# Optimization experiments

Measured on AMD Instinct MI355X. Metric: run time of the kernel, lower is better.

The kernel has to match this reference:

```python
import jax, jax.numpy as jnp
import numpy as np

D_MODEL = 768
NHEAD = 12
D_K = D_MODEL // NHEAD
D_FF = 3072
EPS = 1e-6


def layer_norm(x, a, b):
    # torch LayerNorm here: mean/std over last dim, std is UNBIASED (n-1), eps added to std
    n = x.shape[-1]
    m = jnp.mean(x, axis=-1, keepdims=True)
    var = jnp.sum((x - m) ** 2, axis=-1, keepdims=True) / (n - 1)
    return a * (x - m) / (jnp.sqrt(var) + EPS) + b


def setup_inputs() -> dict:
    key = jax.random.key(0)
    ks = jax.random.split(key, 12)
    B, S = 2, 2048
    s = 1.0 / np.sqrt(D_MODEL)
    inp = {
        'x': jax.random.normal(ks[0], (B, S, D_MODEL), jnp.float32),
        'mask': jnp.ones((B, 1, S), jnp.int32),
        'Wq': jax.random.normal(ks[1], (D_MODEL, D_MODEL), jnp.float32) * s,
        'bq': jnp.zeros((D_MODEL,), jnp.float32),
        'Wk': jax.random.normal(ks[2], (D_MODEL, D_MODEL), jnp.float32) * s,
        'bk': jnp.zeros((D_MODEL,), jnp.float32),
        'Wv': jax.random.normal(ks[3], (D_MODEL, D_MODEL), jnp.float32) * s,
        'bv': jnp.zeros((D_MODEL,), jnp.float32),
        'Wo': jax.random.normal(ks[4], (D_MODEL, D_MODEL), jnp.float32) * s,
        'bo': jnp.zeros((D_MODEL,), jnp.float32),
        'ln1_a': jnp.ones((D_MODEL,), jnp.float32),
        'ln1_b': jnp.zeros((D_MODEL,), jnp.float32),
        'W1': jax.random.normal(ks[5], (D_MODEL, D_FF), jnp.float32) * s,
        'b1': jnp.zeros((D_FF,), jnp.float32),
        'W2': jax.random.normal(ks[6], (D_FF, D_MODEL), jnp.float32) * (1.0 / np.sqrt(D_FF)),
        'b2': jnp.zeros((D_MODEL,), jnp.float32),
        'ln2_a': jnp.ones((D_MODEL,), jnp.float32),
        'ln2_b': jnp.zeros((D_MODEL,), jnp.float32),
    }
    return inp


def reference(x, mask, Wq, bq, Wk, bk, Wv, bv, Wo, bo, ln1_a, ln1_b, W1, b1, W2, b2, ln2_a, ln2_b):
    B, S, _ = x.shape
    # --- sublayer 1: pre-norm self-attention + residual (dropout = eval/no-op) ---
    h = layer_norm(x, ln1_a, ln1_b)
    q = (h @ Wq + bq).reshape(B, S, NHEAD, D_K).transpose(0, 2, 1, 3)  # [B,H,S,Dk]
    k = (h @ Wk + bk).reshape(B, S, NHEAD, D_K).transpose(0, 2, 1, 3)
    v = (h @ Wv + bv).reshape(B, S, NHEAD, D_K).transpose(0, 2, 1, 3)
    scores = jnp.einsum('bhqd,bhkd->bhqk', q, k) / np.sqrt(D_K)  # [B,H,S,S]
    scores = jnp.where(mask[:, None] == 0, jnp.float32(-1e9), scores)
    attn = jax.nn.softmax(scores, axis=-1)
    ctx = jnp.einsum('bhqk,bhkd->bhqd', attn, v)  # [B,H,S,Dk]
    ctx = ctx.transpose(0, 2, 1, 3).reshape(B, S, D_MODEL)
    x = x + (ctx @ Wo + bo)
    # --- sublayer 2: pre-norm FFN + residual ---
    h2 = layer_norm(x, ln2_a, ln2_b)
    ff = jax.nn.relu(h2 @ W1 + b1) @ W2 + b2
    return x + ff
```

## Files before the change

kernel.cpp:

```cpp
#include <hip/hip_runtime.h>
#include <hip/hip_bf16.h>
#include <stdint.h>

#define DM 768
#define DFF 3072
#define NH 12
#define DK 64
#define SS 2048
#define NTOK 4096

typedef __hip_bfloat16 bf16;
typedef short bf16x8 __attribute__((ext_vector_type(8)));
typedef float f32x4 __attribute__((ext_vector_type(4)));

#define MFMA16(a, b, c) __builtin_amdgcn_mfma_f32_16x16x32_bf16((a), (b), (c), 0, 0, 0)

static __device__ __forceinline__ bf16 f2b(float f) { return __float2bfloat16(f); }
static __device__ __forceinline__ unsigned short f2b_bits(float f) {
    bf16 h = __float2bfloat16(f);
    return *reinterpret_cast<unsigned short*>(&h);
}

static __device__ __forceinline__ void g2l16(const void* g, void* l) {
    __builtin_amdgcn_global_load_lds(
        (const __attribute__((address_space(1))) unsigned int*)g,
        (__attribute__((address_space(3))) unsigned int*)(uintptr_t)l,
        16, 0, 0);
}

__global__ __launch_bounds__(256) void transpose_cvt(const float* __restrict__ W,
                                                     bf16* __restrict__ WT,
                                                     int K, int N) {
    __shared__ float tile[32][33];
    int n0 = blockIdx.x * 32, k0 = blockIdx.y * 32;
    int tx = threadIdx.x & 31, ty = threadIdx.x >> 5;
#pragma unroll
    for (int r = ty; r < 32; r += 8)
        tile[r][tx] = W[(size_t)(k0 + r) * N + n0 + tx];
    __syncthreads();
#pragma unroll
    for (int r = ty; r < 32; r += 8)
        WT[(size_t)(n0 + r) * K + k0 + tx] = f2b(tile[tx][r]);
}

__global__ __launch_bounds__(256) void transpose_cvt4(const float* W0, const float* W1,
                                                      const float* W2, const float* W3,
                                                      bf16* T0, bf16* T1, bf16* T2, bf16* T3) {
    __shared__ float tile[32][33];
    const float* W = (blockIdx.z == 0) ? W0 : (blockIdx.z == 1) ? W1 : (blockIdx.z == 2) ? W2 : W3;
    bf16* WT = (blockIdx.z == 0) ? T0 : (blockIdx.z == 1) ? T1 : (blockIdx.z == 2) ? T2 : T3;
    int n0 = blockIdx.x * 32, k0 = blockIdx.y * 32;
    int tx = threadIdx.x & 31, ty = threadIdx.x >> 5;
#pragma unroll
    for (int r = ty; r < 32; r += 8)
        tile[r][tx] = W[(size_t)(k0 + r) * DM + n0 + tx];
    __syncthreads();
#pragma unroll
    for (int r = ty; r < 32; r += 8)
        WT[(size_t)(n0 + r) * DM + k0 + tx] = f2b(tile[tx][r]);
}

__global__ __launch_bounds__(256) void ln_fwd(const float* __restrict__ x,
                                              const float* __restrict__ g,
                                              const float* __restrict__ be,
                                              bf16* __restrict__ out) {
    int wid = threadIdx.x >> 6, lane = threadIdx.x & 63;
    int row = blockIdx.x * 4 + wid;
    const float* xr = x + (size_t)row * DM;
    float v[12];
    float s = 0.f;
#pragma unroll
    for (int i = 0; i < 12; ++i) { v[i] = xr[lane + i * 64]; s += v[i]; }
#pragma unroll
    for (int off = 32; off >= 1; off >>= 1) s += __shfl_xor(s, off);
    float mean = s * (1.f / 768.f);
    float s2 = 0.f;
#pragma unroll
    for (int i = 0; i < 12; ++i) { float d = v[i] - mean; s2 += d * d; }
#pragma unroll
    for (int off = 32; off >= 1; off >>= 1) s2 += __shfl_xor(s2, off);
    float rstd = 1.f / (sqrtf(s2 * (1.f / 767.f)) + 1e-6f);
    bf16* orow = out + (size_t)row * DM;
#pragma unroll
    for (int i = 0; i < 12; ++i) {
        int c = lane + i * 64;
        orow[c] = f2b(g[c] * (v[i] - mean) * rstd + be[c]);
    }
}

__device__ __forceinline__ void gemm_core(const bf16* __restrict__ A,
                                          const bf16* __restrict__ BT,
                                          int K, int bm, int bn,
                                          bf16* As, bf16* Bs,
                                          f32x4 acc[4][4]) {
    int tid = threadIdx.x;
    int lane = tid & 63, quad = lane >> 4, lid = lane & 15;
    int wid = tid >> 6;
    int wm = (wid >> 1) * 64, wn = (wid & 1) * 64;
    int s0 = tid, s1 = tid + 256;
    int r0 = s0 >> 2, c0 = (s0 & 3) ^ ((r0 >> 1) & 3);
    int r1 = s1 >> 2, c1 = (s1 & 3) ^ ((r1 >> 1) & 3);
    const bf16* A0 = A + (size_t)(bm + r0) * K + c0 * 8;
    const bf16* A1 = A + (size_t)(bm + r1) * K + c1 * 8;
    const bf16* B0 = BT + (size_t)(bn + r0) * K + c0 * 8;
    const bf16* B1 = BT + (size_t)(bn + r1) * K + c1 * 8;
    int rdc = quad ^ ((lid >> 1) & 3);
    for (int k0 = 0; k0 < K; k0 += 32) {
        __syncthreads();
        g2l16(A0 + k0, As + s0 * 8);
        g2l16(B0 + k0, Bs + s0 * 8);
        g2l16(A1 + k0, As + s1 * 8);
        g2l16(B1 + k0, Bs + s1 * 8);
        __syncthreads();
        bf16x8 af[4], bfr[4];
#pragma unroll
        for (int i = 0; i < 4; ++i) af[i]  = *(const bf16x8*)&As[(wm + i * 16 + lid) * 32 + rdc * 8];
#pragma unroll
        for (int j = 0; j < 4; ++j) bfr[j] = *(const bf16x8*)&Bs[(wn + j * 16 + lid) * 32 + rdc * 8];
#pragma unroll
        for (int i = 0; i < 4; ++i)
#pragma unroll
            for (int j = 0; j < 4; ++j)
                acc[i][j] = MFMA16(af[i], bfr[j], acc[i][j]);
    }
}

__global__ __launch_bounds__(256) void gemm_qkv(const bf16* __restrict__ A,
                                                const bf16* __restrict__ WqT,
                                                const bf16* __restrict__ WkT,
                                                const bf16* __restrict__ WvT,
                                                const float* __restrict__ bq,
                                                const float* __restrict__ bk,
                                                const float* __restrict__ bv,
                                                bf16* __restrict__ qb,
                                                bf16* __restrict__ kb,
                                                bf16* __restrict__ vtb) {
    __shared__ bf16 As[128 * 32];
    __shared__ bf16 Bs[128 * 32];
    int which = blockIdx.x / 6;
    int bn = (blockIdx.x % 6) * 128;
    int bm = blockIdx.y * 128;
    const bf16* BT = (which == 0) ? WqT : (which == 1) ? WkT : WvT;
    const float* bias = (which == 0) ? bq : (which == 1) ? bk : bv;
    f32x4 acc[4][4] = {};
    gemm_core(A, BT, DM, bm, bn, As, Bs, acc);

    int tid = threadIdx.x, wid = tid >> 6, lane = tid & 63, quad = lane >> 4, lid = lane & 15;
    int wm = (wid >> 1) * 64, wn = (wid & 1) * 64;
#pragma unroll
    for (int j = 0; j < 4; ++j) {
        int col = bn + wn + j * 16 + lid;
        float bb = bias[col];
        int hh = col >> 6, d = col & 63;
#pragma unroll
        for (int i = 0; i < 4; ++i) {
            int rowbase = bm + wm + i * 16 + quad * 4;
            int b = rowbase >> 11;
            int s0 = rowbase & 2047;
            if (which == 2) {
                ushort4 pk;
                pk.x = f2b_bits(acc[i][j][0] + bb);
                pk.y = f2b_bits(acc[i][j][1] + bb);
                pk.z = f2b_bits(acc[i][j][2] + bb);
                pk.w = f2b_bits(acc[i][j][3] + bb);
                *(ushort4*)&vtb[(((size_t)b * NH + hh) * DK + d) * SS + s0] = pk;
            } else {
                bf16* dst = which ? kb : qb;
#pragma unroll
                for (int r = 0; r < 4; ++r)
                    dst[(((size_t)b * NH + hh) * SS + (s0 + r)) * DK + d] = f2b(acc[i][j][r] + bb);
            }
        }
    }
}

template <int EPI>
__global__ __launch_bounds__(256) void gemm_ep(const bf16* __restrict__ A,
                                               const bf16* __restrict__ BT,
                                               const float* __restrict__ bias,
                                               const float* __restrict__ res,
                                               void* __restrict__ outp,
                                               int N, int K) {
    __shared__ bf16 As[128 * 32];
    __shared__ bf16 Bs[128 * 32];
    int bm = blockIdx.y * 128, bn = blockIdx.x * 128;
    f32x4 acc[4][4] = {};
    gemm_core(A, BT, K, bm, bn, As, Bs, acc);

    int tid = threadIdx.x, wid = tid >> 6, lane = tid & 63, quad = lane >> 4, lid = lane & 15;
    int wm = (wid >> 1) * 64, wn = (wid & 1) * 64;
#pragma unroll
    for (int j = 0; j < 4; ++j) {
        int col = bn + wn + j * 16 + lid;
        float bb = bias[col];
#pragma unroll
        for (int i = 0; i < 4; ++i) {
#pragma unroll
            for (int r = 0; r < 4; ++r) {
                int row = bm + wm + i * 16 + quad * 4 + r;
                float v = acc[i][j][r] + bb;
                if (EPI == 2) {
                    ((float*)outp)[(size_t)row * N + col] = res[(size_t)row * N + col] + v;
                } else {
                    ((bf16*)outp)[(size_t)row * N + col] = f2b(fmaxf(v, 0.f));
                }
            }
        }
    }
}

template <int EPI>
__global__ __launch_bounds__(256) void gemm_ep64(const bf16* __restrict__ A,
                                                 const bf16* __restrict__ BT,
                                                 const float* __restrict__ bias,
                                                 const float* __restrict__ res,
                                                 void* __restrict__ outp,
                                                 int N, int K) {
    __shared__ bf16 As[64 * 32];
    __shared__ bf16 Bs[128 * 32];
    int bm = blockIdx.y * 64, bn = blockIdx.x * 128;
    int tid = threadIdx.x, wid = tid >> 6, lane = tid & 63, quad = lane >> 4, lid = lane & 15;
    int wm = (wid >> 1) * 32, wn = (wid & 1) * 64;
    f32x4 acc[2][4] = {};
    int ra = tid >> 2, ca = (tid & 3) ^ ((ra >> 1) & 3);
    int s0 = tid, s1 = tid + 256;
    int rb0 = s0 >> 2, cb0 = (s0 & 3) ^ ((rb0 >> 1) & 3);
    int rb1 = s1 >> 2, cb1 = (s1 & 3) ^ ((rb1 >> 1) & 3);
    const bf16* Ap = A + (size_t)(bm + ra) * K + ca * 8;
    const bf16* B0 = BT + (size_t)(bn + rb0) * K + cb0 * 8;
    const bf16* B1 = BT + (size_t)(bn + rb1) * K + cb1 * 8;
    int rdc = quad ^ ((lid >> 1) & 3);
    for (int k0 = 0; k0 < K; k0 += 32) {
        __syncthreads();
        g2l16(Ap + k0, As + tid * 8);
        g2l16(B0 + k0, Bs + s0 * 8);
        g2l16(B1 + k0, Bs + s1 * 8);
        __syncthreads();
        bf16x8 af[2], bfr[4];
#pragma unroll
        for (int i = 0; i < 2; ++i) af[i]  = *(const bf16x8*)&As[(wm + i * 16 + lid) * 32 + rdc * 8];
#pragma unroll
        for (int j = 0; j < 4; ++j) bfr[j] = *(const bf16x8*)&Bs[(wn + j * 16 + lid) * 32 + rdc * 8];
#pragma unroll
        for (int i = 0; i < 2; ++i)
#pragma unroll
            for (int j = 0; j < 4; ++j)
                acc[i][j] = MFMA16(af[i], bfr[j], acc[i][j]);
    }
#pragma unroll
    for (int j = 0; j < 4; ++j) {
        int col = bn + wn + j * 16 + lid;
        float bb = bias[col];
#pragma unroll
        for (int i = 0; i < 2; ++i) {
#pragma unroll
            for (int r = 0; r < 4; ++r) {
                int row = bm + wm + i * 16 + quad * 4 + r;
                float v = acc[i][j][r] + bb;
                if (EPI == 2) {
                    ((float*)outp)[(size_t)row * N + col] = res[(size_t)row * N + col] + v;
                } else {
                    ((bf16*)outp)[(size_t)row * N + col] = f2b(fmaxf(v, 0.f));
                }
            }
        }
    }
}

__global__ __launch_bounds__(256) void attn_fwd(const bf16* __restrict__ qb,
                                                const bf16* __restrict__ kb,
                                                const bf16* __restrict__ vtb,
                                                const int* __restrict__ mask,
                                                bf16* __restrict__ ctx) {
    __shared__ bf16 Qs[64 * 64];
    __shared__ bf16 Ks[2][64 * 64];
    __shared__ bf16 VTs[2][64 * 64];
    __shared__ bf16 Ps[64 * 72];
    int bh = blockIdx.y;
    int b = bh / NH, h = bh % NH;
    int q0 = blockIdx.x * 64;
    const bf16* Q  = qb  + (size_t)bh * SS * DK;
    const bf16* Kp = kb  + (size_t)bh * SS * DK;
    const bf16* VT = vtb + (size_t)bh * DK * SS;
    int tid = threadIdx.x, wid = tid >> 6, lane = tid & 63, quad = lane >> 4, lid = lane & 15;

    int s0 = tid, s1 = tid + 256;
    int r0 = s0 >> 3, c0 = (s0 & 7) ^ (r0 & 7);
    int r1 = s1 >> 3, c1 = (s1 & 7) ^ (r1 & 7);
    g2l16(Q + (size_t)(q0 + r0) * DK + c0 * 8, Qs + s0 * 8);
    g2l16(Q + (size_t)(q0 + r1) * DK + c1 * 8, Qs + s1 * 8);
    g2l16(Kp + (size_t)r0 * DK + c0 * 8, Ks[0] + s0 * 8);
    g2l16(Kp + (size_t)r1 * DK + c1 * 8, Ks[0] + s1 * 8);
    g2l16(VT + (size_t)r0 * SS + c0 * 8, VTs[0] + s0 * 8);
    g2l16(VT + (size_t)r1 * SS + c1 * 8, VTs[0] + s1 * 8);

    int rdc  = quad ^ (lid & 7);
    int rdc2 = rdc ^ 4;

    f32x4 accv[4] = {};
    float l_part[4] = {0.f, 0.f, 0.f, 0.f};

    for (int t = 0; t < SS / 64; ++t) {
        __syncthreads();
        int cur = t & 1;
        if (t + 1 < SS / 64) {
            int k1 = (t + 1) * 64;
            g2l16(Kp + (size_t)(k1 + r0) * DK + c0 * 8, Ks[cur ^ 1] + s0 * 8);
            g2l16(Kp + (size_t)(k1 + r1) * DK + c1 * 8, Ks[cur ^ 1] + s1 * 8);
            g2l16(VT + (size_t)r0 * SS + k1 + c0 * 8, VTs[cur ^ 1] + s0 * 8);
            g2l16(VT + (size_t)r1 * SS + k1 + c1 * 8, VTs[cur ^ 1] + s1 * 8);
        }
        int k0 = t * 64;
        const bf16* Kc = Ks[cur];
        const bf16* Vc = VTs[cur];

        int mk[4];
#pragma unroll
        for (int ns = 0; ns < 4; ++ns) mk[ns] = mask[b * SS + k0 + ns * 16 + lid];

#pragma unroll
        for (int ns = 0; ns < 4; ++ns) {
            f32x4 sa = {};
            sa = MFMA16(*(const bf16x8*)&Qs[(wid * 16 + lid) * 64 + rdc * 8],
                        *(const bf16x8*)&Kc[(ns * 16 + lid) * 64 + rdc * 8], sa);
            sa = MFMA16(*(const bf16x8*)&Qs[(wid * 16 + lid) * 64 + rdc2 * 8],
                        *(const bf16x8*)&Kc[(ns * 16 + lid) * 64 + rdc2 * 8], sa);
#pragma unroll
            for (int r = 0; r < 4; ++r) {
                float pv = mk[ns] ? __expf(sa[r] * 0.125f) : 0.f;
                Ps[(wid * 16 + quad * 4 + r) * 72 + ns * 16 + lid] = f2b(pv);
                l_part[r] += pv;
            }
        }

#pragma unroll
        for (int ds = 0; ds < 4; ++ds) {
            accv[ds] = MFMA16(*(const bf16x8*)&Ps[(wid * 16 + lid) * 72 + quad * 8],
                              *(const bf16x8*)&Vc[(ds * 16 + lid) * 64 + rdc * 8], accv[ds]);
            accv[ds] = MFMA16(*(const bf16x8*)&Ps[(wid * 16 + lid) * 72 + 32 + quad * 8],
                              *(const bf16x8*)&Vc[(ds * 16 + lid) * 64 + rdc2 * 8], accv[ds]);
        }
    }

#pragma unroll
    for (int r = 0; r < 4; ++r) {
#pragma unroll
        for (int off = 8; off >= 1; off >>= 1) l_part[r] += __shfl_xor(l_part[r], off);
    }

#pragma unroll
    for (int ds = 0; ds < 4; ++ds) {
#pragma unroll
        for (int r = 0; r < 4; ++r) {
            int row = q0 + wid * 16 + quad * 4 + r;
            int col = h * DK + ds * 16 + lid;
            ctx[(size_t)(b * SS + row) * DM + col] = f2b(accv[ds][r] / l_part[r]);
        }
    }
}

extern "C" void kernel_launch(void* const* d_in, const int* in_sizes, int n_in,
                              void* d_out, int out_size, void* d_ws, size_t ws_size,
                              hipStream_t stream) {
    const float* x    = (const float*)d_in[0];
    const int*   mask = (const int*)d_in[1];
    const float* Wq   = (const float*)d_in[2];
    const float* bq   = (const float*)d_in[3];
    const float* Wk   = (const float*)d_in[4];
    const float* bk   = (const float*)d_in[5];
    const float* Wv   = (const float*)d_in[6];
    const float* bv   = (const float*)d_in[7];
    const float* Wo   = (const float*)d_in[8];
    const float* bo   = (const float*)d_in[9];
    const float* ln1a = (const float*)d_in[10];
    const float* ln1b = (const float*)d_in[11];
    const float* W1   = (const float*)d_in[12];
    const float* b1   = (const float*)d_in[13];
    const float* W2   = (const float*)d_in[14];
    const float* b2   = (const float*)d_in[15];
    const float* ln2a = (const float*)d_in[16];
    const float* ln2b = (const float*)d_in[17];
    float* out = (float*)d_out;

    char* w = (char*)d_ws;
    bf16* h   = (bf16*)w; w += (size_t)NTOK * DM * 2;
    bf16* qb  = (bf16*)w; w += (size_t)NTOK * DM * 2;
    bf16* kb  = (bf16*)w; w += (size_t)NTOK * DM * 2;
    bf16* vtb = (bf16*)w; w += (size_t)NTOK * DM * 2;
    bf16* ctx = (bf16*)w; w += (size_t)NTOK * DM * 2;
    bf16* h2  = (bf16*)w; w += (size_t)NTOK * DM * 2;
    bf16* ffa = (bf16*)w; w += (size_t)NTOK * DFF * 2;
    float* x1 = (float*)w; w += (size_t)NTOK * DM * 4;
    bf16* WqT = (bf16*)w; w += (size_t)DM * DM * 2;
    bf16* WkT = (bf16*)w; w += (size_t)DM * DM * 2;
    bf16* WvT = (bf16*)w; w += (size_t)DM * DM * 2;
    bf16* WoT = (bf16*)w; w += (size_t)DM * DM * 2;
    bf16* W1T = (bf16*)w; w += (size_t)DM * DFF * 2;
    bf16* W2T = (bf16*)w; w += (size_t)DM * DFF * 2;

    transpose_cvt4<<<dim3(24, 24, 4), 256, 0, stream>>>(Wq, Wk, Wv, Wo, WqT, WkT, WvT, WoT);
    transpose_cvt<<<dim3(96, 24), 256, 0, stream>>>(W1, W1T, DM, DFF);
    transpose_cvt<<<dim3(24, 96), 256, 0, stream>>>(W2, W2T, DFF, DM);

    ln_fwd<<<NTOK / 4, 256, 0, stream>>>(x, ln1a, ln1b, h);
    gemm_qkv<<<dim3(18, 32), 256, 0, stream>>>(h, WqT, WkT, WvT, bq, bk, bv, qb, kb, vtb);
    attn_fwd<<<dim3(SS / 64, 2 * NH), 256, 0, stream>>>(qb, kb, vtb, mask, ctx);
    gemm_ep64<2><<<dim3(6, 64), 256, 0, stream>>>(ctx, WoT, bo, x, (void*)x1, DM, DM);
    ln_fwd<<<NTOK / 4, 256, 0, stream>>>(x1, ln2a, ln2b, h2);
    gemm_ep<3><<<dim3(24, 32), 256, 0, stream>>>(h2, W1T, b1, nullptr, (void*)ffa, DFF, DM);
    gemm_ep64<2><<<dim3(6, 64), 256, 0, stream>>>(ffa, W2T, b2, x1, (void*)out, DM, DFF);
}
```

Before: 319.4 us.

## Double-buffer GEMM LDS tiles and keep attention probabilities in registers

The GEMM cores now double-buffer their shared-memory tiles, prefetching the next K slice while computing the current one, which drops one barrier per iteration. The attention kernel computes transposed scores (K·Qᵀ) so the probability fragments land directly in the B-operand layout of a 16x16x16 MFMA. This removes the P round-trip through LDS. Q is pre-scaled by log2(e)/sqrt(dk) in the QKV epilogue so exp2f replaces expf plus a multiply. LDS usage for the GEMMs doubles, which may lower occupancy, and the attention path depends on a K16 bf16 MFMA builtin being available.

```diff
diff --git a/kernel.cpp b/kernel.cpp
--- a/kernel.cpp
+++ b/kernel.cpp
@@ -10,10 +10,23 @@
 #define NTOK 4096
 
 typedef __hip_bfloat16 bf16;
+typedef short bf16x4 __attribute__((ext_vector_type(4)));
 typedef short bf16x8 __attribute__((ext_vector_type(8)));
 typedef float f32x4 __attribute__((ext_vector_type(4)));
 
 #define MFMA16(a, b, c) __builtin_amdgcn_mfma_f32_16x16x32_bf16((a), (b), (c), 0, 0, 0)
+
+#if __has_builtin(__builtin_amdgcn_mfma_f32_16x16x16bf16_1k)
+#define HAVE_K16 1
+#define MFMA_K16(a, b, c) __builtin_amdgcn_mfma_f32_16x16x16bf16_1k((a), (b), (c), 0, 0, 0)
+#elif __has_builtin(__builtin_amdgcn_mfma_f32_16x16x16_bf16)
+#define HAVE_K16 1
+#define MFMA_K16(a, b, c) __builtin_amdgcn_mfma_f32_16x16x16_bf16((a), (b), (c), 0, 0, 0)
+#else
+#define HAVE_K16 0
+#endif
+
+#define QSCALE 0.18033688011112042f
 
 static __device__ __forceinline__ bf16 f2b(float f) { return __float2bfloat16(f); }
 static __device__ __forceinline__ unsigned short f2b_bits(float f) {
@@ -105,18 +118,27 @@
     const bf16* B0 = BT + (size_t)(bn + r0) * K + c0 * 8;
     const bf16* B1 = BT + (size_t)(bn + r1) * K + c1 * 8;
     int rdc = quad ^ ((lid >> 1) & 3);
+    g2l16(A0, As + s0 * 8);
+    g2l16(B0, Bs + s0 * 8);
+    g2l16(A1, As + s1 * 8);
+    g2l16(B1, Bs + s1 * 8);
     for (int k0 = 0; k0 < K; k0 += 32) {
         __syncthreads();
-        g2l16(A0 + k0, As + s0 * 8);
-        g2l16(B0 + k0, Bs + s0 * 8);
-        g2l16(A1 + k0, As + s1 * 8);
-        g2l16(B1 + k0, Bs + s1 * 8);
-        __syncthreads();
+        int cur = (k0 >> 5) & 1;
+        if (k0 + 32 < K) {
+            int nb = (cur ^ 1) * 4096;
+            g2l16(A0 + k0 + 32, As + nb + s0 * 8);
+            g2l16(B0 + k0 + 32, Bs + nb + s0 * 8);
+            g2l16(A1 + k0 + 32, As + nb + s1 * 8);
+            g2l16(B1 + k0 + 32, Bs + nb + s1 * 8);
+        }
+        const bf16* Ac = As + cur * 4096;
+        const bf16* Bc = Bs + cur * 4096;
         bf16x8 af[4], bfr[4];
 #pragma unroll
-        for (int i = 0; i < 4; ++i) af[i]  = *(const bf16x8*)&As[(wm + i * 16 + lid) * 32 + rdc * 8];
-#pragma unroll
-        for (int j = 0; j < 4; ++j) bfr[j] = *(const bf16x8*)&Bs[(wn + j * 16 + lid) * 32 + rdc * 8];
+        for (int i = 0; i < 4; ++i) af[i]  = *(const bf16x8*)&Ac[(wm + i * 16 + lid) * 32 + rdc * 8];
+#pragma unroll
+        for (int j = 0; j < 4; ++j) bfr[j] = *(const bf16x8*)&Bc[(wn + j * 16 + lid) * 32 + rdc * 8];
 #pragma unroll
         for (int i = 0; i < 4; ++i)
 #pragma unroll
@@ -135,8 +157,8 @@
                                                 bf16* __restrict__ qb,
                                                 bf16* __restrict__ kb,
                                                 bf16* __restrict__ vtb) {
-    __shared__ bf16 As[128 * 32];
-    __shared__ bf16 Bs[128 * 32];
+    __shared__ bf16 As[2 * 128 * 32];
+    __shared__ bf16 Bs[2 * 128 * 32];
     int which = blockIdx.x / 6;
     int bn = (blockIdx.x % 6) * 128;
     int bm = blockIdx.y * 128;
@@ -147,6 +169,7 @@
 
     int tid = threadIdx.x, wid = tid >> 6, lane = tid & 63, quad = lane >> 4, lid = lane & 15;
     int wm = (wid >> 1) * 64, wn = (wid & 1) * 64;
+    float sc = (which == 0) ? QSCALE : 1.f;
 #pragma unroll
     for (int j = 0; j < 4; ++j) {
         int col = bn + wn + j * 16 + lid;
@@ -168,7 +191,7 @@
                 bf16* dst = which ? kb : qb;
 #pragma unroll
                 for (int r = 0; r < 4; ++r)
-                    dst[(((size_t)b * NH + hh) * SS + (s0 + r)) * DK + d] = f2b(acc[i][j][r] + bb);
+                    dst[(((size_t)b * NH + hh) * SS + (s0 + r)) * DK + d] = f2b((acc[i][j][r] + bb) * sc);
             }
         }
     }
@@ -181,8 +204,8 @@
                                                const float* __restrict__ res,
                                                void* __restrict__ outp,
                                                int N, int K) {
-    __shared__ bf16 As[128 * 32];
-    __shared__ bf16 Bs[128 * 32];
+    __shared__ bf16 As[2 * 128 * 32];
+    __shared__ bf16 Bs[2 * 128 * 32];
     int bm = blockIdx.y * 128, bn = blockIdx.x * 128;
     f32x4 acc[4][4] = {};
     gemm_core(A, BT, K, bm, bn, As, Bs, acc);
@@ -216,8 +239,8 @@
                                                  const float* __restrict__ res,
                                                  void* __restrict__ outp,
                                                  int N, int K) {
-    __shared__ bf16 As[64 * 32];
-    __shared__ bf16 Bs[128 * 32];
+    __shared__ bf16 As[2 * 64 * 32];
+    __shared__ bf16 Bs[2 * 128 * 32];
     int bm = blockIdx.y * 64, bn = blockIdx.x * 128;
     int tid = threadIdx.x, wid = tid >> 6, lane = tid & 63, quad = lane >> 4, lid = lane & 15;
     int wm = (wid >> 1) * 32, wn = (wid & 1) * 64;
@@ -230,17 +253,24 @@
     const bf16* B0 = BT + (size_t)(bn + rb0) * K + cb0 * 8;
     const bf16* B1 = BT + (size_t)(bn + rb1) * K + cb1 * 8;
     int rdc = quad ^ ((lid >> 1) & 3);
+    g2l16(Ap, As + tid * 8);
+    g2l16(B0, Bs + s0 * 8);
+    g2l16(B1, Bs + s1 * 8);
     for (int k0 = 0; k0 < K; k0 += 32) {
         __syncthreads();
-        g2l16(Ap + k0, As + tid * 8);
-        g2l16(B0 + k0, Bs + s0 * 8);
-        g2l16(B1 + k0, Bs + s1 * 8);
-        __syncthreads();
+        int cur = (k0 >> 5) & 1;
+        if (k0 + 32 < K) {
+            g2l16(Ap + k0 + 32, As + (cur ^ 1) * 2048 + tid * 8);
+            g2l16(B0 + k0 + 32, Bs + (cur ^ 1) * 4096 + s0 * 8);
+            g2l16(B1 + k0 + 32, Bs + (cur ^ 1) * 4096 + s1 * 8);
+        }
+        const bf16* Ac = As + cur * 2048;
+        const bf16* Bc = Bs + cur * 4096;
         bf16x8 af[2], bfr[4];
 #pragma unroll
-        for (int i = 0; i < 2; ++i) af[i]  = *(const bf16x8*)&As[(wm + i * 16 + lid) * 32 + rdc * 8];
-#pragma unroll
-        for (int j = 0; j < 4; ++j) bfr[j] = *(const bf16x8*)&Bs[(wn + j * 16 + lid) * 32 + rdc * 8];
+        for (int i = 0; i < 2; ++i) af[i]  = *(const bf16x8*)&Ac[(wm + i * 16 + lid) * 32 + rdc * 8];
+#pragma unroll
+        for (int j = 0; j < 4; ++j) bfr[j] = *(const bf16x8*)&Bc[(wn + j * 16 + lid) * 32 + rdc * 8];
 #pragma unroll
         for (int i = 0; i < 2; ++i)
 #pragma unroll
@@ -267,12 +297,106 @@
     }
 }
 
+#if HAVE_K16
 __global__ __launch_bounds__(256) void attn_fwd(const bf16* __restrict__ qb,
                                                 const bf16* __restrict__ kb,
                                                 const bf16* __restrict__ vtb,
                                                 const int* __restrict__ mask,
                                                 bf16* __restrict__ ctx) {
-    __shared__ bf16 Qs[64 * 64];
+    __shared__ bf16 Ks[2][64 * 64];
+    __shared__ bf16 VTs[2][64 * 64];
+    int bh = blockIdx.y;
+    int b = bh / NH, h = bh % NH;
+    int q0 = blockIdx.x * 64;
+    const bf16* Q  = qb  + (size_t)bh * SS * DK;
+    const bf16* Kp = kb  + (size_t)bh * SS * DK;
+    const bf16* VT = vtb + (size_t)bh * DK * SS;
+    int tid = threadIdx.x, wid = tid >> 6, lane = tid & 63, quad = lane >> 4, lid = lane & 15;
+
+    int s0 = tid, s1 = tid + 256;
+    int r0 = s0 >> 3, c0 = (s0 & 7) ^ (r0 & 7);
+    int r1 = s1 >> 3, c1 = (s1 & 7) ^ (r1 & 7);
+    g2l16(Kp + (size_t)r0 * DK + c0 * 8, Ks[0] + s0 * 8);
+    g2l16(Kp + (size_t)r1 * DK + c1 * 8, Ks[0] + s1 * 8);
+    g2l16(VT + (size_t)r0 * SS + c0 * 8, VTs[0] + s0 * 8);
+    g2l16(VT + (size_t)r1 * SS + c1 * 8, VTs[0] + s1 * 8);
+
+    const bf16* Qrow = Q + (size_t)(q0 + wid * 16 + lid) * DK;
+    bf16x8 qf0 = *(const bf16x8*)&Qrow[quad * 8];
+    bf16x8 qf1 = *(const bf16x8*)&Qrow[32 + quad * 8];
+
+    int rdc  = quad ^ (lid & 7);
+    int rdc2 = rdc ^ 4;
+    const int* mrow = mask + b * SS;
+
+    f32x4 accv[4] = {};
+    float l_part = 0.f;
+
+    for (int t = 0; t < SS / 64; ++t) {
+        __syncthreads();
+        int cur = t & 1;
+        if (t + 1 < SS / 64) {
+            int k1 = (t + 1) * 64;
+            g2l16(Kp + (size_t)(k1 + r0) * DK + c0 * 8, Ks[cur ^ 1] + s0 * 8);
+            g2l16(Kp + (size_t)(k1 + r1) * DK + c1 * 8, Ks[cur ^ 1] + s1 * 8);
+            g2l16(VT + (size_t)r0 * SS + k1 + c0 * 8, VTs[cur ^ 1] + s0 * 8);
+            g2l16(VT + (size_t)r1 * SS + k1 + c1 * 8, VTs[cur ^ 1] + s1 * 8);
+        }
+        int k0 = t * 64;
+        const bf16* Kc = Ks[cur];
+        const bf16* Vc = VTs[cur];
+
+        bf16x4 pf[4];
+#pragma unroll
+        for (int ns = 0; ns < 4; ++ns) {
+            f32x4 st = {};
+            st = MFMA16(*(const bf16x8*)&Kc[(ns * 16 + lid) * 64 + rdc * 8],  qf0, st);
+            st = MFMA16(*(const bf16x8*)&Kc[(ns * 16 + lid) * 64 + rdc2 * 8], qf1, st);
+            int4 mk = *(const int4*)&mrow[k0 + ns * 16 + quad * 4];
+            float p0 = mk.x ? exp2f(st[0]) : 0.f;
+            float p1 = mk.y ? exp2f(st[1]) : 0.f;
+            float p2 = mk.z ? exp2f(st[2]) : 0.f;
+            float p3 = mk.w ? exp2f(st[3]) : 0.f;
+            l_part += (p0 + p1) + (p2 + p3);
+            bf16x4 pv;
+            pv[0] = (short)f2b_bits(p0);
+            pv[1] = (short)f2b_bits(p1);
+            pv[2] = (short)f2b_bits(p2);
+            pv[3] = (short)f2b_bits(p3);
+            pf[ns] = pv;
+        }
+
+#pragma unroll
+        for (int ds = 0; ds < 4; ++ds) {
+#pragma unroll
+            for (int ns = 0; ns < 4; ++ns) {
+                int pc = (2 * ns + (quad >> 1)) ^ (lid & 7);
+                bf16x4 vf = *(const bf16x4*)&Vc[(ds * 16 + lid) * 64 + pc * 8 + (quad & 1) * 4];
+                accv[ds] = MFMA_K16(vf, pf[ns], accv[ds]);
+            }
+        }
+    }
+
+    l_part += __shfl_xor(l_part, 16);
+    l_part += __shfl_xor(l_part, 32);
+    float rl = 1.f / l_part;
+
+#pragma unroll
+    for (int ds = 0; ds < 4; ++ds) {
+        ushort4 pk;
+        pk.x = f2b_bits(accv[ds][0] * rl);
+        pk.y = f2b_bits(accv[ds][1] * rl);
+        pk.z = f2b_bits(accv[ds][2] * rl);
+        pk.w = f2b_bits(accv[ds][3] * rl);
+        *(ushort4*)&ctx[(size_t)(b * SS + q0 + wid * 16 + lid) * DM + h * DK + ds * 16 + quad * 4] = pk;
+    }
+}
+#else
+__global__ __launch_bounds__(256) void attn_fwd(const bf16* __restrict__ qb,
+                                                const bf16* __restrict__ kb,
+                                                const bf16* __restrict__ vtb,
+                                                const int* __restrict__ mask,
+                                                bf16* __restrict__ ctx) {
     __shared__ bf16 Ks[2][64 * 64];
     __shared__ bf16 VTs[2][64 * 64];
     __shared__ bf16 Ps[64 * 72];
@@ -283,23 +407,20 @@
     const bf16* Kp = kb  + (size_t)bh * SS * DK;
     const bf16* VT = vtb + (size_t)bh * DK * SS;
     int tid = threadIdx.x, wid = tid >> 6, lane = tid & 63, quad = lane >> 4, lid = lane & 15;
-
     int s0 = tid, s1 = tid + 256;
     int r0 = s0 >> 3, c0 = (s0 & 7) ^ (r0 & 7);
     int r1 = s1 >> 3, c1 = (s1 & 7) ^ (r1 & 7);
-    g2l16(Q + (size_t)(q0 + r0) * DK + c0 * 8, Qs + s0 * 8);
-    g2l16(Q + (size_t)(q0 + r1) * DK + c1 * 8, Qs + s1 * 8);
     g2l16(Kp + (size_t)r0 * DK + c0 * 8, Ks[0] + s0 * 8);
     g2l16(Kp + (size_t)r1 * DK + c1 * 8, Ks[0] + s1 * 8);
     g2l16(VT + (size_t)r0 * SS + c0 * 8, VTs[0] + s0 * 8);
     g2l16(VT + (size_t)r1 * SS + c1 * 8, VTs[0] + s1 * 8);
-
+    const bf16* Qrow = Q + (size_t)(q0 + wid * 16 + lid) * DK;
+    bf16x8 qf0 = *(const bf16x8*)&Qrow[quad * 8];
+    bf16x8 qf1 = *(const bf16x8*)&Qrow[32 + quad * 8];
     int rdc  = quad ^ (lid & 7);
     int rdc2 = rdc ^ 4;
-
     f32x4 accv[4] = {};
     float l_part[4] = {0.f, 0.f, 0.f, 0.f};
-
     for (int t = 0; t < SS / 64; ++t) {
         __syncthreads();
         int cur = t & 1;
@@ -313,26 +434,21 @@
         int k0 = t * 64;
         const bf16* Kc = Ks[cur];
         const bf16* Vc = VTs[cur];
-
         int mk[4];
 #pragma unroll
         for (int ns = 0; ns < 4; ++ns) mk[ns] = mask[b * SS + k0 + ns * 16 + lid];
-
 #pragma unroll
         for (int ns = 0; ns < 4; ++ns) {
             f32x4 sa = {};
-            sa = MFMA16(*(const bf16x8*)&Qs[(wid * 16 + lid) * 64 + rdc * 8],
-                        *(const bf16x8*)&Kc[(ns * 16 + lid) * 64 + rdc * 8], sa);
-            sa = MFMA16(*(const bf16x8*)&Qs[(wid * 16 + lid) * 64 + rdc2 * 8],
-                        *(const bf16x8*)&Kc[(ns * 16 + lid) * 64 + rdc2 * 8], sa);
+            sa = MFMA16(qf0, *(const bf16x8*)&Kc[(ns * 16 + lid) * 64 + rdc * 8], sa);
+            sa = MFMA16(qf1, *(const bf16x8*)&Kc[(ns * 16 + lid) * 64 + rdc2 * 8], sa);
 #pragma unroll
             for (int r = 0; r < 4; ++r) {
-                float pv = mk[ns] ? __expf(sa[r] * 0.125f) : 0.f;
+                float pv = mk[ns] ? exp2f(sa[r]) : 0.f;
                 Ps[(wid * 16 + quad * 4 + r) * 72 + ns * 16 + lid] = f2b(pv);
                 l_part[r] += pv;
             }
         }
-
 #pragma unroll
         for (int ds = 0; ds < 4; ++ds) {
             accv[ds] = MFMA16(*(const bf16x8*)&Ps[(wid * 16 + lid) * 72 + quad * 8],
@@ -341,13 +457,11 @@
                               *(const bf16x8*)&Vc[(ds * 16 + lid) * 64 + rdc2 * 8], accv[ds]);
         }
     }
-
 #pragma unroll
     for (int r = 0; r < 4; ++r) {
 #pragma unroll
         for (int off = 8; off >= 1; off >>= 1) l_part[r] += __shfl_xor(l_part[r], off);
     }
-
 #pragma unroll
     for (int ds = 0; ds < 4; ++ds) {
 #pragma unroll
@@ -358,6 +472,7 @@
         }
     }
 }
+#endif
 
 extern "C" void kernel_launch(void* const* d_in, const int* in_sizes, int n_in,
                               void* d_out, int out_size, void* d_ws, size_t ws_size,
```

After: 320.9 us. About the same (+0.5%).

## Split attention over key chunks, double-buffer GEMM tiles, fold softmax scale into Q

Applied to the files above, without the earlier changes.

Attention is split into four key-range chunks. Each chunk block writes unnormalized bf16 partial context and row sums into scratch space reused from the FFN and x1 buffers. A new combine kernel then sums the partials and normalizes. This multiplies the attention grid to expose more parallelism, at the cost of an extra kernel and significant partial-result memory traffic. All GEMM cores now double-buffer LDS tiles and use one barrier per k-step so global-to-LDS loads overlap MFMA work. The 1/sqrt(dk)*log2(e) factor is folded into Q at the QKV epilogue so attention can use exp2f, and Q fragments are held in registers instead of LDS.

```diff
diff --git a/kernel.cpp b/kernel.cpp
--- a/kernel.cpp
+++ b/kernel.cpp
@@ -8,18 +8,22 @@
 #define DK 64
 #define SS 2048
 #define NTOK 4096
+#define KCH 4
 
 typedef __hip_bfloat16 bf16;
 typedef short bf16x8 __attribute__((ext_vector_type(8)));
 typedef float f32x4 __attribute__((ext_vector_type(4)));
 
 #define MFMA16(a, b, c) __builtin_amdgcn_mfma_f32_16x16x32_bf16((a), (b), (c), 0, 0, 0)
+
+#define QSCALE 0.18033688011112042f
 
 static __device__ __forceinline__ bf16 f2b(float f) { return __float2bfloat16(f); }
 static __device__ __forceinline__ unsigned short f2b_bits(float f) {
     bf16 h = __float2bfloat16(f);
     return *reinterpret_cast<unsigned short*>(&h);
 }
+static __device__ __forceinline__ float b2f(bf16 h) { return __bfloat162float(h); }
 
 static __device__ __forceinline__ void g2l16(const void* g, void* l) {
     __builtin_amdgcn_global_load_lds(
@@ -105,18 +109,27 @@
     const bf16* B0 = BT + (size_t)(bn + r0) * K + c0 * 8;
     const bf16* B1 = BT + (size_t)(bn + r1) * K + c1 * 8;
     int rdc = quad ^ ((lid >> 1) & 3);
+    g2l16(A0, As + s0 * 8);
+    g2l16(B0, Bs + s0 * 8);
+    g2l16(A1, As + s1 * 8);
+    g2l16(B1, Bs + s1 * 8);
     for (int k0 = 0; k0 < K; k0 += 32) {
         __syncthreads();
-        g2l16(A0 + k0, As + s0 * 8);
-        g2l16(B0 + k0, Bs + s0 * 8);
-        g2l16(A1 + k0, As + s1 * 8);
-        g2l16(B1 + k0, Bs + s1 * 8);
-        __syncthreads();
+        int cur = (k0 >> 5) & 1;
+        if (k0 + 32 < K) {
+            int nb = (cur ^ 1) * 4096;
+            g2l16(A0 + k0 + 32, As + nb + s0 * 8);
+            g2l16(B0 + k0 + 32, Bs + nb + s0 * 8);
+            g2l16(A1 + k0 + 32, As + nb + s1 * 8);
+            g2l16(B1 + k0 + 32, Bs + nb + s1 * 8);
+        }
+        const bf16* Ac = As + cur * 4096;
+        const bf16* Bc = Bs + cur * 4096;
         bf16x8 af[4], bfr[4];
 #pragma unroll
-        for (int i = 0; i < 4; ++i) af[i]  = *(const bf16x8*)&As[(wm + i * 16 + lid) * 32 + rdc * 8];
-#pragma unroll
-        for (int j = 0; j < 4; ++j) bfr[j] = *(const bf16x8*)&Bs[(wn + j * 16 + lid) * 32 + rdc * 8];
+        for (int i = 0; i < 4; ++i) af[i]  = *(const bf16x8*)&Ac[(wm + i * 16 + lid) * 32 + rdc * 8];
+#pragma unroll
+        for (int j = 0; j < 4; ++j) bfr[j] = *(const bf16x8*)&Bc[(wn + j * 16 + lid) * 32 + rdc * 8];
 #pragma unroll
         for (int i = 0; i < 4; ++i)
 #pragma unroll
@@ -135,8 +148,8 @@
                                                 bf16* __restrict__ qb,
                                                 bf16* __restrict__ kb,
                                                 bf16* __restrict__ vtb) {
-    __shared__ bf16 As[128 * 32];
-    __shared__ bf16 Bs[128 * 32];
+    __shared__ bf16 As[2 * 128 * 32];
+    __shared__ bf16 Bs[2 * 128 * 32];
     int which = blockIdx.x / 6;
     int bn = (blockIdx.x % 6) * 128;
     int bm = blockIdx.y * 128;
@@ -147,6 +160,7 @@
 
     int tid = threadIdx.x, wid = tid >> 6, lane = tid & 63, quad = lane >> 4, lid = lane & 15;
     int wm = (wid >> 1) * 64, wn = (wid & 1) * 64;
+    float sc = (which == 0) ? QSCALE : 1.f;
 #pragma unroll
     for (int j = 0; j < 4; ++j) {
         int col = bn + wn + j * 16 + lid;
@@ -168,7 +182,7 @@
                 bf16* dst = which ? kb : qb;
 #pragma unroll
                 for (int r = 0; r < 4; ++r)
-                    dst[(((size_t)b * NH + hh) * SS + (s0 + r)) * DK + d] = f2b(acc[i][j][r] + bb);
+                    dst[(((size_t)b * NH + hh) * SS + (s0 + r)) * DK + d] = f2b((acc[i][j][r] + bb) * sc);
             }
         }
     }
@@ -181,8 +195,8 @@
                                                const float* __restrict__ res,
                                                void* __restrict__ outp,
                                                int N, int K) {
-    __shared__ bf16 As[128 * 32];
-    __shared__ bf16 Bs[128 * 32];
+    __shared__ bf16 As[2 * 128 * 32];
+    __shared__ bf16 Bs[2 * 128 * 32];
     int bm = blockIdx.y * 128, bn = blockIdx.x * 128;
     f32x4 acc[4][4] = {};
     gemm_core(A, BT, K, bm, bn, As, Bs, acc);
@@ -216,8 +230,8 @@
                                                  const float* __restrict__ res,
                                                  void* __restrict__ outp,
                                                  int N, int K) {
-    __shared__ bf16 As[64 * 32];
-    __shared__ bf16 Bs[128 * 32];
+    __shared__ bf16 As[2 * 64 * 32];
+    __shared__ bf16 Bs[2 * 128 * 32];
     int bm = blockIdx.y * 64, bn = blockIdx.x * 128;
     int tid = threadIdx.x, wid = tid >> 6, lane = tid & 63, quad = lane >> 4, lid = lane & 15;
     int wm = (wid >> 1) * 32, wn = (wid & 1) * 64;
@@ -230,17 +244,24 @@
     const bf16* B0 = BT + (size_t)(bn + rb0) * K + cb0 * 8;
     const bf16* B1 = BT + (size_t)(bn + rb1) * K + cb1 * 8;
     int rdc = quad ^ ((lid >> 1) & 3);
+    g2l16(Ap, As + tid * 8);
+    g2l16(B0, Bs + s0 * 8);
+    g2l16(B1, Bs + s1 * 8);
     for (int k0 = 0; k0 < K; k0 += 32) {
         __syncthreads();
-        g2l16(Ap + k0, As + tid * 8);
-        g2l16(B0 + k0, Bs + s0 * 8);
-        g2l16(B1 + k0, Bs + s1 * 8);
-        __syncthreads();
+        int cur = (k0 >> 5) & 1;
+        if (k0 + 32 < K) {
+            g2l16(Ap + k0 + 32, As + (cur ^ 1) * 2048 + tid * 8);
+            g2l16(B0 + k0 + 32, Bs + (cur ^ 1) * 4096 + s0 * 8);
+            g2l16(B1 + k0 + 32, Bs + (cur ^ 1) * 4096 + s1 * 8);
+        }
+        const bf16* Ac = As + cur * 2048;
+        const bf16* Bc = Bs + cur * 4096;
         bf16x8 af[2], bfr[4];
 #pragma unroll
-        for (int i = 0; i < 2; ++i) af[i]  = *(const bf16x8*)&As[(wm + i * 16 + lid) * 32 + rdc * 8];
-#pragma unroll
-        for (int j = 0; j < 4; ++j) bfr[j] = *(const bf16x8*)&Bs[(wn + j * 16 + lid) * 32 + rdc * 8];
+        for (int i = 0; i < 2; ++i) af[i]  = *(const bf16x8*)&Ac[(wm + i * 16 + lid) * 32 + rdc * 8];
+#pragma unroll
+        for (int j = 0; j < 4; ++j) bfr[j] = *(const bf16x8*)&Bc[(wn + j * 16 + lid) * 32 + rdc * 8];
 #pragma unroll
         for (int i = 0; i < 2; ++i)
 #pragma unroll
@@ -267,18 +288,19 @@
     }
 }
 
-__global__ __launch_bounds__(256) void attn_fwd(const bf16* __restrict__ qb,
-                                                const bf16* __restrict__ kb,
-                                                const bf16* __restrict__ vtb,
-                                                const int* __restrict__ mask,
-                                                bf16* __restrict__ ctx) {
-    __shared__ bf16 Qs[64 * 64];
-    __shared__ bf16 Ks[2][64 * 64];
-    __shared__ bf16 VTs[2][64 * 64];
+__global__ __launch_bounds__(256) void attn_part(const bf16* __restrict__ qb,
+                                                 const bf16* __restrict__ kb,
+                                                 const bf16* __restrict__ vtb,
+                                                 const int* __restrict__ mask,
+                                                 bf16* __restrict__ part,
+                                                 float* __restrict__ lws) {
+    __shared__ bf16 Ks[64 * 64];
+    __shared__ bf16 VTs[64 * 64];
     __shared__ bf16 Ps[64 * 72];
     int bh = blockIdx.y;
     int b = bh / NH, h = bh % NH;
     int q0 = blockIdx.x * 64;
+    int kc = blockIdx.z;
     const bf16* Q  = qb  + (size_t)bh * SS * DK;
     const bf16* Kp = kb  + (size_t)bh * SS * DK;
     const bf16* VT = vtb + (size_t)bh * DK * SS;
@@ -287,47 +309,39 @@
     int s0 = tid, s1 = tid + 256;
     int r0 = s0 >> 3, c0 = (s0 & 7) ^ (r0 & 7);
     int r1 = s1 >> 3, c1 = (s1 & 7) ^ (r1 & 7);
-    g2l16(Q + (size_t)(q0 + r0) * DK + c0 * 8, Qs + s0 * 8);
-    g2l16(Q + (size_t)(q0 + r1) * DK + c1 * 8, Qs + s1 * 8);
-    g2l16(Kp + (size_t)r0 * DK + c0 * 8, Ks[0] + s0 * 8);
-    g2l16(Kp + (size_t)r1 * DK + c1 * 8, Ks[0] + s1 * 8);
-    g2l16(VT + (size_t)r0 * SS + c0 * 8, VTs[0] + s0 * 8);
-    g2l16(VT + (size_t)r1 * SS + c1 * 8, VTs[0] + s1 * 8);
+
+    const bf16* Qrow = Q + (size_t)(q0 + wid * 16 + lid) * DK;
+    bf16x8 qf0 = *(const bf16x8*)&Qrow[quad * 8];
+    bf16x8 qf1 = *(const bf16x8*)&Qrow[32 + quad * 8];
 
     int rdc  = quad ^ (lid & 7);
     int rdc2 = rdc ^ 4;
+    const int* mrow = mask + b * SS;
 
     f32x4 accv[4] = {};
     float l_part[4] = {0.f, 0.f, 0.f, 0.f};
 
-    for (int t = 0; t < SS / 64; ++t) {
+    for (int t = kc * (SS / 64 / KCH); t < (kc + 1) * (SS / 64 / KCH); ++t) {
+        int k0 = t * 64;
         __syncthreads();
-        int cur = t & 1;
-        if (t + 1 < SS / 64) {
-            int k1 = (t + 1) * 64;
-            g2l16(Kp + (size_t)(k1 + r0) * DK + c0 * 8, Ks[cur ^ 1] + s0 * 8);
-            g2l16(Kp + (size_t)(k1 + r1) * DK + c1 * 8, Ks[cur ^ 1] + s1 * 8);
-            g2l16(VT + (size_t)r0 * SS + k1 + c0 * 8, VTs[cur ^ 1] + s0 * 8);
-            g2l16(VT + (size_t)r1 * SS + k1 + c1 * 8, VTs[cur ^ 1] + s1 * 8);
-        }
-        int k0 = t * 64;
-        const bf16* Kc = Ks[cur];
-        const bf16* Vc = VTs[cur];
+        g2l16(Kp + (size_t)(k0 + r0) * DK + c0 * 8, Ks + s0 * 8);
+        g2l16(Kp + (size_t)(k0 + r1) * DK + c1 * 8, Ks + s1 * 8);
+        g2l16(VT + (size_t)r0 * SS + k0 + c0 * 8, VTs + s0 * 8);
+        g2l16(VT + (size_t)r1 * SS + k0 + c1 * 8, VTs + s1 * 8);
+        __syncthreads();
 
         int mk[4];
 #pragma unroll
-        for (int ns = 0; ns < 4; ++ns) mk[ns] = mask[b * SS + k0 + ns * 16 + lid];
+        for (int ns = 0; ns < 4; ++ns) mk[ns] = mrow[k0 + ns * 16 + lid];
 
 #pragma unroll
         for (int ns = 0; ns < 4; ++ns) {
             f32x4 sa = {};
-            sa = MFMA16(*(const bf16x8*)&Qs[(wid * 16 + lid) * 64 + rdc * 8],
-                        *(const bf16x8*)&Kc[(ns * 16 + lid) * 64 + rdc * 8], sa);
-            sa = MFMA16(*(const bf16x8*)&Qs[(wid * 16 + lid) * 64 + rdc2 * 8],
-                        *(const bf16x8*)&Kc[(ns * 16 + lid) * 64 + rdc2 * 8], sa);
+            sa = MFMA16(qf0, *(const bf16x8*)&Ks[(ns * 16 + lid) * 64 + rdc * 8], sa);
+            sa = MFMA16(qf1, *(const bf16x8*)&Ks[(ns * 16 + lid) * 64 + rdc2 * 8], sa);
 #pragma unroll
             for (int r = 0; r < 4; ++r) {
-                float pv = mk[ns] ? __expf(sa[r] * 0.125f) : 0.f;
+                float pv = mk[ns] ? exp2f(sa[r]) : 0.f;
                 Ps[(wid * 16 + quad * 4 + r) * 72 + ns * 16 + lid] = f2b(pv);
                 l_part[r] += pv;
             }
@@ -336,9 +350,9 @@
 #pragma unroll
         for (int ds = 0; ds < 4; ++ds) {
             accv[ds] = MFMA16(*(const bf16x8*)&Ps[(wid * 16 + lid) * 72 + quad * 8],
-                              *(const bf16x8*)&Vc[(ds * 16 + lid) * 64 + rdc * 8], accv[ds]);
+                              *(const bf16x8*)&VTs[(ds * 16 + lid) * 64 + rdc * 8], accv[ds]);
             accv[ds] = MFMA16(*(const bf16x8*)&Ps[(wid * 16 + lid) * 72 + 32 + quad * 8],
-                              *(const bf16x8*)&Vc[(ds * 16 + lid) * 64 + rdc2 * 8], accv[ds]);
+                              *(const bf16x8*)&VTs[(ds * 16 + lid) * 64 + rdc2 * 8], accv[ds]);
         }
     }
 
@@ -346,6 +360,11 @@
     for (int r = 0; r < 4; ++r) {
 #pragma unroll
         for (int off = 8; off >= 1; off >>= 1) l_part[r] += __shfl_xor(l_part[r], off);
+    }
+    if (lid == 0) {
+#pragma unroll
+        for (int r = 0; r < 4; ++r)
+            lws[((size_t)kc * (2 * NH) + bh) * SS + q0 + wid * 16 + quad * 4 + r] = l_part[r];
     }
 
 #pragma unroll
@@ -354,9 +373,26 @@
         for (int r = 0; r < 4; ++r) {
             int row = q0 + wid * 16 + quad * 4 + r;
             int col = h * DK + ds * 16 + lid;
-            ctx[(size_t)(b * SS + row) * DM + col] = f2b(accv[ds][r] / l_part[r]);
-        }
-    }
+            part[((size_t)kc * NTOK + b * SS + row) * DM + col] = f2b(accv[ds][r]);
+        }
+    }
+}
+
+__global__ __launch_bounds__(256) void attn_combine(const bf16* __restrict__ part,
+                                                    const float* __restrict__ lws,
+                                                    bf16* __restrict__ ctx) {
+    int c = blockIdx.x * 256 + threadIdx.x;
+    int t = blockIdx.y;
+    int h = c >> 6;
+    int b = t >> 11, q = t & 2047;
+    int bh = b * NH + h;
+    float s = 0.f, l = 0.f;
+#pragma unroll
+    for (int kc = 0; kc < KCH; ++kc) {
+        s += b2f(part[((size_t)kc * NTOK + t) * DM + c]);
+        l += lws[((size_t)kc * (2 * NH) + bh) * SS + q];
+    }
+    ctx[(size_t)t * DM + c] = f2b(s / l);
 }
 
 extern "C" void kernel_launch(void* const* d_in, const int* in_sizes, int n_in,
@@ -398,13 +434,17 @@
     bf16* W1T = (bf16*)w; w += (size_t)DM * DFF * 2;
     bf16* W2T = (bf16*)w; w += (size_t)DM * DFF * 2;
 
+    bf16*  part = ffa;
+    float* lws  = x1;
+
     transpose_cvt4<<<dim3(24, 24, 4), 256, 0, stream>>>(Wq, Wk, Wv, Wo, WqT, WkT, WvT, WoT);
     transpose_cvt<<<dim3(96, 24), 256, 0, stream>>>(W1, W1T, DM, DFF);
     transpose_cvt<<<dim3(24, 96), 256, 0, stream>>>(W2, W2T, DFF, DM);
 
     ln_fwd<<<NTOK / 4, 256, 0, stream>>>(x, ln1a, ln1b, h);
     gemm_qkv<<<dim3(18, 32), 256, 0, stream>>>(h, WqT, WkT, WvT, bq, bk, bv, qb, kb, vtb);
-    attn_fwd<<<dim3(SS / 64, 2 * NH), 256, 0, stream>>>(qb, kb, vtb, mask, ctx);
+    attn_part<<<dim3(SS / 64, 2 * NH, KCH), 256, 0, stream>>>(qb, kb, vtb, mask, part, lws);
+    attn_combine<<<dim3(DM / 256, NTOK), 256, 0, stream>>>(part, lws, ctx);
     gemm_ep64<2><<<dim3(6, 64), 256, 0, stream>>>(ctx, WoT, bo, x, (void*)x1, DM, DM);
     ln_fwd<<<NTOK / 4, 256, 0, stream>>>(x1, ln2a, ln2b, h2);
     gemm_ep<3><<<dim3(24, 32), 256, 0, stream>>>(h2, W1T, b1, nullptr, (void*)ffa, DFF, DM);
```

Result: faster. 310.7 us (-2.7%).
